# Performance work log

Measured on AMD Instinct MI355X. Metric: run time of the kernel, lower is better.

## Reference

```python
import jax, jax.numpy as jnp
import numpy as np

N, D, KF, KN = 256, 32, 16, 50       # neurons, state dim, feature dim, top-k neighbors
GAMMA, LAM_A, DT, STEPS = 0.1, 0.95, 0.05, 20
B, UIN = 512, 128                    # batch, input feature dim


def _safe_norm(x):
    # L2 norm over last dim; eps keeps the gradient finite at x=0 (torch's subgradient is 0 there)
    return jnp.sqrt(jnp.sum(x * x, axis=-1) + 1e-12)


def setup_inputs() -> dict:
    key = jax.random.key(0)
    ks = jax.random.split(key, 6)
    return {
        'u': jax.random.normal(ks[0], (B, N, UIN), jnp.float32),
        'features': jax.random.normal(ks[1], (N, KF), jnp.float32),
        'bias': jnp.zeros((N, D), jnp.float32),
        'w_in': jax.random.normal(ks[2], (D, UIN), jnp.float32) * 0.05,
        'b_in': jnp.zeros((D,), jnp.float32),
        'sig_w1': jax.random.normal(ks[3], (16, 1), jnp.float32) * 0.25,
        'sig_b1': jnp.zeros((16,), jnp.float32),
        'sig_w2': jax.random.normal(ks[4], (D, 16), jnp.float32) * 0.25,
        'sig_b2': jnp.zeros((D,), jnp.float32),
    }


def reference(u, features, bias, w_in, b_in, sig_w1, sig_b1, sig_w2, sig_b2):
    # --- top-k sparse similarity (computed once, reused across all 20 steps) ---
    f = features / jnp.linalg.norm(features, axis=1, keepdims=True)
    sim = f @ f.T                                   # [N, N]
    vals, idx = jax.lax.top_k(sim, KN)              # [N, KN] each; idx is the sparse pattern

    u_proj = u @ w_in.T + b_in                      # [B, N, D], loop-invariant
    x0 = jnp.zeros((u.shape[0], N, D), u.dtype)
    ab0 = jnp.zeros((u.shape[0], N), u.dtype)

    def step(carry, _):
        x, a_bar = carry
        a = jnp.tanh(_safe_norm(x))                 # [B, N] firing rates
        # sparse neighbor aggregation: gather top-KN neighbor activities, weighted sum
        syn = jnp.einsum('bnk,nk->bn', a[:, idx], vals)   # [B, N]
        # sigma MLP: Linear(1,16) -> GELU(exact) -> Linear(16,D)
        h = jax.nn.gelu(syn[..., None] * sig_w1[:, 0] + sig_b1, approximate=False)
        h = h @ sig_w2.T + sig_b2                   # [B, N, D]
        dx = -GAMMA * x + h + bias + u_proj
        x = x + DT * dx
        a_bar = LAM_A * a_bar + (1.0 - LAM_A) * jnp.tanh(_safe_norm(x))
        return (x, a_bar), None

    (x, _), _ = jax.lax.scan(step, (x0, ab0), None, length=STEPS)
    return x
```

## Files before the change

kernel.cpp:

```cpp
#include <hip/hip_runtime.h>
#include <math.h>

#define N_NEU 256
#define D_DIM 32
#define KFD   16
#define KN    50
#define B_SZ  512
#define UINF  128
#define GAMMA 0.1f
#define DT    0.05f
#define NSTEP 20

#define TBL_K   4096
#define TBL_LO  (-64.0f)
#define TBL_IDL 32.0f

#define TOPK_BLKS  N_NEU
#define TBL_BLKS   (TBL_K * 16 / 256)

typedef __attribute__((ext_vector_type(8))) short bf16x8;
typedef __attribute__((ext_vector_type(4))) float f32x4;

__device__ __forceinline__ unsigned short f2bf(float f) {
    unsigned u = __float_as_uint(f);
    u += 0x7FFFu + ((u >> 16) & 1u);
    return (unsigned short)(u >> 16);
}
__device__ __forceinline__ float bf_lo(unsigned q) { return __uint_as_float(q << 16); }
__device__ __forceinline__ float bf_hi(unsigned q) { return __uint_as_float(q & 0xFFFF0000u); }

__global__ __launch_bounds__(256) void pre_kernel(const float* __restrict__ features,
                                                  const float* __restrict__ sig_w1,
                                                  const float* __restrict__ sig_b1,
                                                  const float* __restrict__ sig_w2,
                                                  int* __restrict__ idxT,
                                                  float* __restrict__ vals2T,
                                                  unsigned int* __restrict__ tblb) {
    __shared__ float fsh[N_NEU][KFD + 1];
    __shared__ float sim_sh[N_NEU];

    const int bid = blockIdx.x;

    if (bid < TOPK_BLKS) {
        const int n = bid;
        const int j = threadIdx.x;

        float v[KFD];
        float s = 0.f;
#pragma unroll
        for (int d = 0; d < KFD; ++d) { v[d] = features[j * KFD + d]; s = fmaf(v[d], v[d], s); }
        const float nrm = sqrtf(s);
#pragma unroll
        for (int d = 0; d < KFD; ++d) fsh[j][d] = v[d] / nrm;
        __syncthreads();

        float dot = 0.f;
#pragma unroll
        for (int d = 0; d < KFD; ++d) dot = fmaf(fsh[n][d], fsh[j][d], dot);
        sim_sh[j] = dot;
        __syncthreads();

        const float my = dot;
        int rank = 0;
#pragma unroll 8
        for (int i = 0; i < N_NEU; ++i) {
            const float si = sim_sh[i];
            rank += (si > my || (si == my && i < j)) ? 1 : 0;
        }
        if (rank < KN) {
            const int s_ = rank / 14;
            const int r_ = rank - 14 * s_;
            vals2T[((r_ >> 1) * 1024 + n * 4 + s_) * 2 + (r_ & 1)] = my;
            idxT[rank * N_NEU + n] = j;
        }
        if (j == 0) {
#pragma unroll
            for (int k = 50; k < 56; ++k) {
                const int r_ = k - 42;
                vals2T[((r_ >> 1) * 1024 + n * 4 + 3) * 2 + (r_ & 1)] = 0.f;
            }
        }
    } else {
        const int gid = (bid - TOPK_BLKS) * 256 + threadIdx.x;
        const int k = gid >> 4, p = gid & 15;
        const int d0 = 2 * p, d1 = 2 * p + 1;
        const float s0 = TBL_LO + (float)k / TBL_IDL;
        float g0 = 0.f, g1 = 0.f;
#pragma unroll
        for (int j = 0; j < 16; ++j) {
            const float w1 = sig_w1[j], b1 = sig_b1[j];
            const float h0 = fmaf(s0, w1, b1);
            const float e0 = 0.5f * h0 * (1.0f + erff(h0 * 0.70710678118654752f));
            g0 = fmaf(e0, sig_w2[d0 * 16 + j], g0);
            g1 = fmaf(e0, sig_w2[d1 * 16 + j], g1);
        }
        g0 *= DT; g1 *= DT;
        tblb[gid] = (unsigned int)f2bf(g0) | ((unsigned int)f2bf(g1) << 16);
    }
}

__global__ __launch_bounds__(1024) void steps_kernel(const float* __restrict__ u,
                                                     const float* __restrict__ w_in,
                                                     const float* __restrict__ b_in,
                                                     const float* __restrict__ bias,
                                                     const float* __restrict__ sig_b2,
                                                     const int* __restrict__ idxT,
                                                     const float* __restrict__ vals2T,
                                                     const unsigned int* __restrict__ tblb,
                                                     float* __restrict__ out) {
    __shared__ unsigned short wsh[32 * 136];
    __shared__ float cdt_sh[2 * 256 * 36];
    __shared__ unsigned int a_sh[2 * N_NEU];

    const int t = threadIdx.x;

    {
        const float4 w4 = reinterpret_cast<const float4*>(w_in)[t];
        const int d = t >> 5, k0 = (t & 31) * 4;
        unsigned short* wp = &wsh[d * 136 + k0];
        wp[0] = f2bf(w4.x); wp[1] = f2bf(w4.y); wp[2] = f2bf(w4.z); wp[3] = f2bf(w4.w);
    }
    __syncthreads();

    {
        const int wave = t >> 6;
        const int lane = t & 63;
        const int row  = lane & 15;
        const int kg   = lane >> 4;
        const int bb0  = wave >> 3;
        const int wrow = (wave & 7) * 32;
        const long bB  = (long)blockIdx.x * 2 + bb0;

        bf16x8 bfrag[2][4];
#pragma unroll
        for (int dt_ = 0; dt_ < 2; ++dt_)
#pragma unroll
            for (int kk = 0; kk < 4; ++kk)
                bfrag[dt_][kk] = *reinterpret_cast<const bf16x8*>(
                    &wsh[(dt_ * 16 + row) * 136 + kk * 32 + kg * 8]);

#pragma unroll
        for (int t4 = 0; t4 < 2; ++t4) {
            const float* ub = u + (bB * N_NEU + wrow + t4 * 16 + row) * UINF + kg * 8;
            float4 L[8];
#pragma unroll
            for (int kk = 0; kk < 4; ++kk) {
                L[kk * 2 + 0] = *reinterpret_cast<const float4*>(ub + kk * 32);
                L[kk * 2 + 1] = *reinterpret_cast<const float4*>(ub + kk * 32 + 4);
            }
            f32x4 a0 = {0.f, 0.f, 0.f, 0.f};
            f32x4 a1 = {0.f, 0.f, 0.f, 0.f};
#pragma unroll
            for (int kk = 0; kk < 4; ++kk) {
                bf16x8 af;
                const float4 x0 = L[kk * 2], x1 = L[kk * 2 + 1];
                af[0] = (short)f2bf(x0.x); af[1] = (short)f2bf(x0.y);
                af[2] = (short)f2bf(x0.z); af[3] = (short)f2bf(x0.w);
                af[4] = (short)f2bf(x1.x); af[5] = (short)f2bf(x1.y);
                af[6] = (short)f2bf(x1.z); af[7] = (short)f2bf(x1.w);
                a0 = __builtin_amdgcn_mfma_f32_16x16x32_bf16(af, bfrag[0][kk], a0, 0, 0, 0);
                a1 = __builtin_amdgcn_mfma_f32_16x16x32_bf16(af, bfrag[1][kk], a1, 0, 0, 0);
            }
            const int   d0   = row;
            const int   d1   = 16 + row;
            const float add0 = b_in[d0] + sig_b2[d0];
            const float add1 = b_in[d1] + sig_b2[d1];
#pragma unroll
            for (int r = 0; r < 4; ++r) {
                const int nl = wrow + t4 * 16 + kg * 4 + r;
                cdt_sh[bb0 * 9216 + nl * 36 + d0] = DT * (a0[r] + add0 + bias[nl * D_DIM + d0]);
                cdt_sh[bb0 * 9216 + nl * 36 + d1] = DT * (a1[r] + add1 + bias[nl * D_DIM + d1]);
            }
        }
    }
    __syncthreads();

    const int n  = t >> 2;
    const int s  = t & 3;
    const int bb = s >> 1;
    const int h  = s & 1;
    const int b  = blockIdx.x * 2 + bb;

    float ccdt[16];
    {
        const float* cbase = &cdt_sh[bb * 9216 + n * 36 + h * 16];
#pragma unroll
        for (int i = 0; i < 4; ++i) {
            const float4 cv = *reinterpret_cast<const float4*>(cbase + i * 4);
            ccdt[4 * i + 0] = cv.x; ccdt[4 * i + 1] = cv.y;
            ccdt[4 * i + 2] = cv.z; ccdt[4 * i + 3] = cv.w;
        }
    }

    const float2* v2g = reinterpret_cast<const float2*>(vals2T);
    float2 vv[7];
#pragma unroll
    for (int jj = 0; jj < 7; ++jj) vv[jj] = v2g[jj * 1024 + t];

    const unsigned int* gp[14];
#pragma unroll
    for (int j = 0; j < 14; ++j) {
        const int k = s * 14 + j;
        const int ii = (k < KN) ? idxT[k * N_NEU + n] : 0;
        gp[j] = &a_sh[ii];
    }

    float x[16];
#pragma unroll
    for (int d = 0; d < 16; ++d) x[d] = 0.f;

    const float K1 = 1.0f - DT * GAMMA;
    const float L2E2 = 2.8853900817779268f;

#define STEP_BODY(BUF)                                                          \
    {                                                                           \
        float nh0 = 0.f, nh1 = 0.f;                                             \
        _Pragma("unroll")                                                       \
        for (int d = 0; d < 16; d += 2) {                                       \
            nh0 = fmaf(x[d], x[d], nh0);                                        \
            nh1 = fmaf(x[d + 1], x[d + 1], nh1);                                \
        }                                                                       \
        const float nh = nh0 + nh1;                                             \
        const float nfull = nh + __shfl_xor(nh, 1, 64) + 1e-12f;                \
        const float z = sqrtf(nfull);                                           \
        const float e2 = __builtin_amdgcn_exp2f(L2E2 * z);                      \
        const float a = fmaf(-2.0f, __builtin_amdgcn_rcpf(e2 + 1.0f), 1.0f);    \
        const float ao = __shfl_xor(a, 2, 64);                                  \
        if (s == 0) a_sh[(BUF) * N_NEU + n] = (unsigned int)f2bf(a) | ((unsigned int)f2bf(ao) << 16); \
        _Pragma("unroll")                                                       \
        for (int d = 0; d < 16; ++d) x[d] = fmaf(K1, x[d], ccdt[d]);            \
        __syncthreads();                                                        \
        float sA0 = 0.f, sA1 = 0.f, sB0 = 0.f, sB1 = 0.f;                       \
        _Pragma("unroll")                                                       \
        for (int jj = 0; jj < 7; ++jj) {                                        \
            const unsigned int p0 = gp[2 * jj][(BUF) * N_NEU];                  \
            const unsigned int p1 = gp[2 * jj + 1][(BUF) * N_NEU];              \
            sA0 = fmaf(bf_lo(p0), vv[jj].x, sA0);                               \
            sB0 = fmaf(bf_hi(p0), vv[jj].x, sB0);                               \
            sA1 = fmaf(bf_lo(p1), vv[jj].y, sA1);                               \
            sB1 = fmaf(bf_hi(p1), vv[jj].y, sB1);                               \
        }                                                                       \
        float sA = sA0 + sA1;                                                   \
        float sB = sB0 + sB1;                                                   \
        sA += __shfl_xor(sA, 1, 64); sA += __shfl_xor(sA, 2, 64);               \
        sB += __shfl_xor(sB, 1, 64); sB += __shfl_xor(sB, 2, 64);               \
        const float syn = bb ? sB : sA;                                         \
        const float uu = fmaf(syn, TBL_IDL, 0.5f - TBL_LO * TBL_IDL);           \
        int i = (int)uu;                                      \
        i = (i < 0) ? 0 : (i > TBL_K - 1 ? TBL_K - 1 : i);                      \
        const uint4* rp = reinterpret_cast<const uint4*>(tblb + (size_t)i * 16 + h * 8); \
        _Pragma("unroll")                                                       \
        for (int c = 0; c < 2; ++c) {                                           \
            const uint4 q = rp[c];                                              \
            x[8 * c + 0] += bf_lo(q.x);                                         \
            x[8 * c + 1] += bf_hi(q.x);                                         \
            x[8 * c + 2] += bf_lo(q.y);                                         \
            x[8 * c + 3] += bf_hi(q.y);                                         \
            x[8 * c + 4] += bf_lo(q.z);                                         \
            x[8 * c + 5] += bf_hi(q.z);                                         \
            x[8 * c + 6] += bf_lo(q.w);                                         \
            x[8 * c + 7] += bf_hi(q.w);                                         \
        }                                                                       \
    }

    for (int it = 0; it < NSTEP / 2; ++it) {
        STEP_BODY(0);
        STEP_BODY(1);
    }
#undef STEP_BODY

    float4* op4 = reinterpret_cast<float4*>(out + ((size_t)b * N_NEU + n) * D_DIM + h * 16);
#pragma unroll
    for (int i = 0; i < 4; ++i)
        op4[i] = make_float4(x[4 * i + 0], x[4 * i + 1], x[4 * i + 2], x[4 * i + 3]);
}

extern "C" void kernel_launch(void* const* d_in, const int* in_sizes, int n_in,
                              void* d_out, int out_size, void* d_ws, size_t ws_size,
                              hipStream_t stream) {
    const float* u        = (const float*)d_in[0];
    const float* features = (const float*)d_in[1];
    const float* bias     = (const float*)d_in[2];
    const float* w_in     = (const float*)d_in[3];
    const float* b_in     = (const float*)d_in[4];
    const float* sig_w1   = (const float*)d_in[5];
    const float* sig_b1   = (const float*)d_in[6];
    const float* sig_w2   = (const float*)d_in[7];
    const float* sig_b2   = (const float*)d_in[8];
    float* out = (float*)d_out;

    char*         ws     = (char*)d_ws;
    int*          idxT   = (int*)ws;
    float*        vals2T = (float*)(ws + 51200);
    unsigned int* tblb   = (unsigned int*)(ws + 108544);

    hipLaunchKernelGGL(pre_kernel, dim3(TOPK_BLKS + TBL_BLKS), dim3(256), 0, stream,
                       features, sig_w1, sig_b1, sig_w2, idxT, vals2T, tblb);
    hipLaunchKernelGGL(steps_kernel, dim3(B_SZ / 2), dim3(1024), 0, stream,
                       u, w_in, b_in, bias, sig_b2, idxT, vals2T, tblb, out);
}
```

Before: 59.93 us.

## Reorder top-k neighbor slots to spread LDS bank accesses in gather

The preprocessing kernel now sorts the selected top-k neighbors by their LDS bank (index mod 32), not by similarity rank. It also rotates the slot assignment by a per-neuron offset and stores the padded entries explicitly. The aim is that the 14 per-thread gathers from the shared activity array hit distinct banks across lanes at each unrolled position, reducing LDS bank conflicts in the 20-step loop. Because the weighted sum is order-invariant, results change only through float summation order. Preprocessing gains an extra O(N) ranking pass per block.

```diff
diff --git a/kernel.cpp b/kernel.cpp
--- a/kernel.cpp
+++ b/kernel.cpp
@@ -33,11 +33,12 @@
                                                   const float* __restrict__ sig_w1,
                                                   const float* __restrict__ sig_b1,
                                                   const float* __restrict__ sig_w2,
-                                                  int* __restrict__ idxT,
+                                                  int* __restrict__ idxS,
                                                   float* __restrict__ vals2T,
                                                   unsigned int* __restrict__ tblb) {
     __shared__ float fsh[N_NEU][KFD + 1];
     __shared__ float sim_sh[N_NEU];
+    __shared__ int   rank_sh[N_NEU];
 
     const int bid = blockIdx.x;
 
@@ -67,18 +68,30 @@
             const float si = sim_sh[i];
             rank += (si > my || (si == my && i < j)) ? 1 : 0;
         }
+        rank_sh[j] = rank;
+        __syncthreads();
+
         if (rank < KN) {
-            const int s_ = rank / 14;
-            const int r_ = rank - 14 * s_;
-            vals2T[((r_ >> 1) * 1024 + n * 4 + s_) * 2 + (r_ & 1)] = my;
-            idxT[rank * N_NEU + n] = j;
-        }
-        if (j == 0) {
-#pragma unroll
-            for (int k = 50; k < 56; ++k) {
-                const int r_ = k - 42;
-                vals2T[((r_ >> 1) * 1024 + n * 4 + 3) * 2 + (r_ & 1)] = 0.f;
+            const int bj = j & 31;
+            int brank = 0;
+#pragma unroll 8
+            for (int i = 0; i < N_NEU; ++i) {
+                const bool sel = rank_sh[i] < KN;
+                const int  bi  = i & 31;
+                brank += (sel && (bi < bj || (bi == bj && i < j))) ? 1 : 0;
             }
+            const int q  = ((brank - 13 * n) % 56 + 56) % 56;
+            const int s_ = q / 14;
+            const int c_ = q - 14 * s_;
+            idxS[q * N_NEU + n] = j;
+            vals2T[((c_ >> 1) * 1024 + n * 4 + s_) * 2 + (c_ & 1)] = my;
+        }
+        if (j < 6) {
+            const int qp = ((50 + j - 13 * n) % 56 + 56) % 56;
+            const int sp = qp / 14;
+            const int cp = qp - 14 * sp;
+            idxS[qp * N_NEU + n] = 0;
+            vals2T[((cp >> 1) * 1024 + n * 4 + sp) * 2 + (cp & 1)] = 0.f;
         }
     } else {
         const int gid = (bid - TOPK_BLKS) * 256 + threadIdx.x;
@@ -104,7 +117,7 @@
                                                      const float* __restrict__ b_in,
                                                      const float* __restrict__ bias,
                                                      const float* __restrict__ sig_b2,
-                                                     const int* __restrict__ idxT,
+                                                     const int* __restrict__ idxS,
                                                      const float* __restrict__ vals2T,
                                                      const unsigned int* __restrict__ tblb,
                                                      float* __restrict__ out) {
@@ -200,8 +213,7 @@
     const unsigned int* gp[14];
 #pragma unroll
     for (int j = 0; j < 14; ++j) {
-        const int k = s * 14 + j;
-        const int ii = (k < KN) ? idxT[k * N_NEU + n] : 0;
+        const int ii = idxS[(s * 14 + j) * N_NEU + n];
         gp[j] = &a_sh[ii];
     }
 
@@ -290,12 +302,12 @@
     float* out = (float*)d_out;
 
     char*         ws     = (char*)d_ws;
-    int*          idxT   = (int*)ws;
-    float*        vals2T = (float*)(ws + 51200);
-    unsigned int* tblb   = (unsigned int*)(ws + 108544);
+    int*          idxS   = (int*)ws;
+    float*        vals2T = (float*)(ws + 57344);
+    unsigned int* tblb   = (unsigned int*)(ws + 114688);
 
     hipLaunchKernelGGL(pre_kernel, dim3(TOPK_BLKS + TBL_BLKS), dim3(256), 0, stream,
-                       features, sig_w1, sig_b1, sig_w2, idxT, vals2T, tblb);
+                       features, sig_w1, sig_b1, sig_w2, idxS, vals2T, tblb);
     hipLaunchKernelGGL(steps_kernel, dim3(B_SZ / 2), dim3(1024), 0, stream,
-                       u, w_in, b_in, bias, sig_b2, idxT, vals2T, tblb, out);
+                       u, w_in, b_in, bias, sig_b2, idxS, vals2T, tblb, out);
 }
```

Result: slower. 67.60 us (+12.8%).
